# Optimization experiments

Measured on AMD Instinct MI355X. Metric: run time of the kernel, lower is better.

The kernel has to match this reference:

```python
import jax, jax.numpy as jnp
import numpy as np

nA = 4096; nB = 4096; C = 128; H = 4; D = 32; E = 65536
EPS = 1e-5


def _ln(x, g, b):
    m = jnp.mean(x, axis=-1, keepdims=True)
    v = jnp.var(x, axis=-1, keepdims=True)
    return (x - m) / jnp.sqrt(v + EPS) * g + b


def setup_inputs() -> dict:
    key = jax.random.key(0)
    ks = jax.random.split(key, 16)
    w = 0.02
    inp = {}
    inp["x_a"] = jax.random.normal(ks[0], (nA, C), dtype=jnp.float32)
    inp["x_b"] = jax.random.normal(ks[1], (nB, C), dtype=jnp.float32)
    inp["edge_ab"] = jax.random.randint(ks[2], (2, E), 0, nA)  # row0: src in A, row1: dst in B
    inp["edge_ba"] = jax.random.randint(ks[3], (2, E), 0, nB)  # row0: src in B, row1: dst in A
    inp["Wq"] = jax.random.normal(ks[4], (C, C), dtype=jnp.float32) * w
    inp["bq"] = jnp.zeros((C,), jnp.float32)
    inp["Wk"] = jax.random.normal(ks[5], (C, C), dtype=jnp.float32) * w
    inp["bk"] = jnp.zeros((C,), jnp.float32)
    inp["Wv"] = jax.random.normal(ks[6], (C, C), dtype=jnp.float32) * w
    inp["bv"] = jnp.zeros((C,), jnp.float32)
    inp["Wo"] = jax.random.normal(ks[7], (C, C), dtype=jnp.float32) * w
    inp["bo"] = jnp.zeros((C,), jnp.float32)
    inp["g_attn"] = jnp.ones((C,), jnp.float32)   # pre_ln_attn
    inp["b_attn"] = jnp.zeros((C,), jnp.float32)
    inp["g_ffn"] = jnp.ones((C,), jnp.float32)    # pre_ln_ffn
    inp["b_ffn"] = jnp.zeros((C,), jnp.float32)
    inp["g_f"] = jnp.ones((C,), jnp.float32)      # LayerNorm inside ffn Sequential
    inp["b_f"] = jnp.zeros((C,), jnp.float32)
    inp["W1"] = jax.random.normal(ks[8], (C, C), dtype=jnp.float32) * w
    inp["b1"] = jnp.zeros((C,), jnp.float32)
    inp["W2"] = jax.random.normal(ks[9], (C, C), dtype=jnp.float32) * w
    inp["b2"] = jnp.zeros((C,), jnp.float32)
    inp["rel_ab"] = jax.random.normal(ks[10], (1,), dtype=jnp.float32)
    inp["rel_ba"] = jax.random.normal(ks[11], (1,), dtype=jnp.float32)
    return inp


def reference(x_a, x_b, edge_ab, edge_ba, Wq, bq, Wk, bk, Wv, bv, Wo, bo,
              g_attn, b_attn, g_ffn, b_ffn, g_f, b_f, W1, b1, W2, b2,
              rel_ab, rel_ba):
    inv_sqrt_d = 1.0 / jnp.sqrt(jnp.float32(D))

    def all_pairs_attn(xq, xkv, rel):
        nQ, nK = xq.shape[0], xkv.shape[0]
        Q = (xq @ Wq + bq).reshape(nQ, H, D)
        K = (xkv @ Wk + bk).reshape(nK, H, D)
        V = (xkv @ Wv + bv).reshape(nK, H, D)
        # [nQ, nK, H] logits with additive relation bias
        logits = jnp.einsum('ihd,jhd->ijh', Q, K) * inv_sqrt_d + rel
        a = jax.nn.softmax(logits, axis=1)  # softmax over all source nodes per dst
        return jnp.einsum('ijh,jhd->ihd', a, V).reshape(nQ, C)

    xn_a = _ln(x_a, g_attn, b_attn)
    xn_b = _ln(x_b, g_attn, b_attn)
    # edge type B->A contributes to dst type A; A->B to dst type B
    attn_a = all_pairs_attn(xn_a, xn_b, rel_ba[0]) @ Wo + bo
    attn_b = all_pairs_attn(xn_b, xn_a, rel_ab[0]) @ Wo + bo

    # total degree = out-degree + in-degree across edge types (eval: dropout = identity)
    ones = jnp.ones((E,), jnp.float32)
    deg_a = jax.ops.segment_sum(ones, edge_ab[0], num_segments=nA) + \
            jax.ops.segment_sum(ones, edge_ba[1], num_segments=nA)
    deg_b = jax.ops.segment_sum(ones, edge_ba[0], num_segments=nB) + \
            jax.ops.segment_sum(ones, edge_ab[1], num_segments=nB)
    attn_a = attn_a + deg_a[:, None]
    attn_b = attn_b + deg_b[:, None]

    res_a = x_a + attn_a
    res_b = x_b + attn_b

    def ffn(xr):
        h = _ln(xr, g_ffn, b_ffn)        # pre_ln_ffn
        h = _ln(h, g_f, b_f)             # LayerNorm inside ffn Sequential
        h = jax.nn.gelu(h @ W1 + b1, approximate=False)
        return h @ W2 + b2

    out_a = res_a + ffn(res_a)
    out_b = res_b + ffn(res_b)
    return jnp.stack([out_a, out_b])  # [2, n, C]
```

## Files before the change

### kernel.cpp

```cpp
#include <hip/hip_runtime.h>

typedef unsigned short u16;
typedef unsigned int   u32;
typedef __attribute__((ext_vector_type(8))) short bf16x8;
typedef __attribute__((ext_vector_type(4))) float f32x4;

#define NEL (8192*128)

#define ASYNC16(ldsptr, gptr) __builtin_amdgcn_global_load_lds( \
    (const __attribute__((address_space(1))) u32*)(gptr), \
    (__attribute__((address_space(3))) u32*)(ldsptr), 16, 0, 0)

__device__ __forceinline__ u16 f2bf(float f){
  u32 u = __builtin_bit_cast(u32, f);
  u = (u + 0x7FFFu + ((u >> 16) & 1u)) >> 16;
  return (u16)u;
}
__device__ __forceinline__ u32 pk2(float a, float b){
  u32 r;
  asm("v_cvt_pk_bf16_f32 %0, %1, %2" : "=v"(r) : "v"(a), "v"(b));
  return r;
}

__global__ __launch_bounds__(256) void prep_kernel(
    const int* __restrict__ eab, const int* __restrict__ eba, float* __restrict__ deg,
    const float* __restrict__ Wq, const float* __restrict__ Wk, const float* __restrict__ Wv,
    const float* __restrict__ Wo, const float* __restrict__ W1, const float* __restrict__ W2,
    u16* __restrict__ WT)
{
  __shared__ float tile[32][33];
  const int b = blockIdx.x, t = threadIdx.x;
  if (b < 256){
    int e = b*256 + t;
    atomicAdd(&deg[eab[e]],              1.f);
    atomicAdd(&deg[4096 + eab[65536+e]], 1.f);
    atomicAdd(&deg[4096 + eba[e]],       1.f);
    atomicAdd(&deg[eba[65536+e]],        1.f);
  } else {
    int id = b - 256;
    int w = id >> 4, tt = id & 15, tr = tt >> 2, tc = tt & 3;
    const float* W = (w==0)?Wq:(w==1)?Wk:(w==2)?Wv:(w==3)?Wo:(w==4)?W1:W2;
    int r = t >> 3, c4 = (t&7)*4;
    float4 v = *(const float4*)(W + (tr*32 + r)*128 + tc*32 + c4);
    tile[r][c4]=v.x; tile[r][c4+1]=v.y; tile[r][c4+2]=v.z; tile[r][c4+3]=v.w;
    __syncthreads();
    int n = t >> 3, k4 = (t&7)*4;
    u32 lo = pk2(tile[k4+0][n], tile[k4+1][n]);
    u32 hi = pk2(tile[k4+2][n], tile[k4+3][n]);
    *(uint2*)(WT + w*16384 + (tc*32+n)*128 + tr*32 + k4) = make_uint2(lo, hi);
  }
}

__global__ __launch_bounds__(256) void ln_qkv_kernel(
    const float* __restrict__ xa, const float* __restrict__ xb,
    const float* __restrict__ g, const float* __restrict__ bvec,
    const u16* __restrict__ WT,
    const float* __restrict__ bq, const float* __restrict__ bk, const float* __restrict__ bv,
    u16* __restrict__ Qb, u16* __restrict__ Kb, u16* __restrict__ VT)
{
  __shared__ float xs[16][132];
  __shared__ __align__(16) u16 abf[16][128];
  __shared__ __align__(16) u16 vtb[128][24];
  const int t = threadIdx.x, lane = t&63, wave = t>>6;
  const int lq = lane&15, lg = lane>>4;
  const int row0 = blockIdx.x*16;
  const float* x = (row0 < 4096) ? (xa + row0*128) : (xb + (row0-4096)*128);
  #pragma unroll
  for (int i=0;i<2;i++){
    int id = t + i*256; int r = id>>5, c4 = (id&31)*4;
    float4 v = *(const float4*)(x + r*128 + c4);
    xs[r][c4]=v.x; xs[r][c4+1]=v.y; xs[r][c4+2]=v.z; xs[r][c4+3]=v.w;
  }
  __syncthreads();
  {
    int r = t>>4, c0 = t&15;
    float s=0.f, s2=0.f;
    #pragma unroll
    for (int j=0;j<8;j++){ float v = xs[r][c0+j*16]; s+=v; s2+=v*v; }
    #pragma unroll
    for (int m=1;m<16;m<<=1){ s += __shfl_xor(s,m); s2 += __shfl_xor(s2,m); }
    float mean = s*0.0078125f;
    float var  = s2*0.0078125f - mean*mean;
    float rstd = rsqrtf(var + 1e-5f);
    #pragma unroll
    for (int j=0;j<8;j++){
      int c = c0 + j*16;
      float h = (xs[r][c]-mean)*rstd*g[c] + bvec[c];
      int sj = (c>>3) ^ (r&7);
      abf[r][sj*8 + (c&7)] = f2bf(h);
    }
  }
  __syncthreads();
  bf16x8 af[4];
  #pragma unroll
  for (int s=0;s<4;s++){
    int sj = (s*4+lg) ^ (lq&7);
    af[s] = *(const bf16x8*)&abf[lq][sj*8];
  }
  const int cb = wave*32;
  const float QSC = 0.17677669529663687f * 1.4426950408889634f;
  #pragma unroll
  for (int m=0;m<3;m++){
    const u16* Wg = WT + m*16384;
    bf16x8 bf[2][4];
    #pragma unroll
    for (int ct=0;ct<2;ct++)
      #pragma unroll
      for (int s=0;s<4;s++)
        bf[ct][s] = *(const bf16x8*)(Wg + (cb+ct*16+lq)*128 + s*32 + lg*8);
    f32x4 acc[2] = {{0,0,0,0},{0,0,0,0}};
    #pragma unroll
    for (int ct=0;ct<2;ct++)
      #pragma unroll
      for (int s=0;s<4;s++)
        acc[ct] = __builtin_amdgcn_mfma_f32_16x16x32_bf16(af[s], bf[ct][s], acc[ct], 0,0,0);
    #pragma unroll
    for (int ct=0;ct<2;ct++){
      int col = cb + ct*16 + lq;
      if (m==0){
        float bb = bq[col];
        #pragma unroll
        for (int r=0;r<4;r++)
          Qb[(row0+4*lg+r)*128 + col] = f2bf((acc[ct][r]+bb)*QSC);
      } else if (m==1){
        float bb = bk[col];
        #pragma unroll
        for (int r=0;r<4;r++)
          Kb[(row0+4*lg+r)*128 + col] = f2bf(acc[ct][r]+bb);
      } else {
        float bb = bv[col];
        #pragma unroll
        for (int r=0;r<4;r++)
          vtb[col][4*lg+r] = f2bf(acc[ct][r]+bb);
      }
    }
  }
  __syncthreads();
  {
    int c = t>>1, half = t&1;
    bf16x8 v = *(const bf16x8*)&vtb[c][half*8];
    *(bf16x8*)(VT + c*8192 + row0 + half*8) = v;
  }
}

__global__ __launch_bounds__(256) void attn_kernel(
    const u16* __restrict__ Qb, const u16* __restrict__ Kb,
    const u16* __restrict__ VT, float* __restrict__ attnraw)
{
  __shared__ __align__(16) u16 Klds[2][4096];
  __shared__ __align__(16) u16 Vlds[2][4096];
  __shared__ __align__(16) u16 Plds[4][2048];
  const int t = threadIdx.x, wave = t>>6, lane = t&63;
  const int lq = lane&15, lg = lane>>4;
  const int h = blockIdx.y, dir = blockIdx.z;
  const int q = blockIdx.x*64 + wave*16 + lq + (dir ? 4096 : 0);
  const int kvb0 = dir ? 0 : 4096;

  bf16x8 qf = *(const bf16x8*)(Qb + q*128 + h*32 + lg*8);
  f32x4 acc0 = {0,0,0,0}, acc1 = {0,0,0,0}, accL = {0,0,0,0};
  bf16x8 ones;
  #pragma unroll
  for (int i=0;i<8;i++) ones[i] = (short)0x3F80;

  const u16* gk = Kb + (kvb0 + (t>>2))*128 + h*32 + (t&3)*8;
  const u16* gv = VT + (h*32 + (t>>4))*8192 + kvb0 + ((t&15)^(t>>4))*8;

  ASYNC16(&Klds[0][t*8],      gk);
  ASYNC16(&Klds[0][t*8+2048], gk + 8192);
  ASYNC16(&Vlds[0][t*8],      gv);
  ASYNC16(&Vlds[0][t*8+2048], gv + 131072);
  asm volatile("s_waitcnt vmcnt(0)" ::: "memory");
  __builtin_amdgcn_s_barrier();

  int cur = 0;
  for (int kt=0; kt<32; ++kt){
    if (kt < 31){
      gk += 16384; gv += 128;
      int nb = cur^1;
      ASYNC16(&Klds[nb][t*8],      gk);
      ASYNC16(&Klds[nb][t*8+2048], gk + 8192);
      ASYNC16(&Vlds[nb][t*8],      gv);
      ASYNC16(&Vlds[nb][t*8+2048], gv + 131072);
    }
    const u16* KL = Klds[cur];
    const u16* VL = Vlds[cur];
    u16* PL = Plds[wave] + lq*128;
    #pragma unroll
    for (int f=0; f<8; ++f){
      bf16x8 kf = *(const bf16x8*)(KL + (f*16+lq)*32 + lg*8);
      f32x4 st = __builtin_amdgcn_mfma_f32_16x16x32_bf16(kf, qf, (f32x4){0.f,0.f,0.f,0.f}, 0,0,0);
      float p0 = __builtin_amdgcn_exp2f(st[0]);
      float p1 = __builtin_amdgcn_exp2f(st[1]);
      float p2 = __builtin_amdgcn_exp2f(st[2]);
      float p3 = __builtin_amdgcn_exp2f(st[3]);
      int j = f*2 + (lg>>1);
      *(uint2*)(PL + ((j ^ lq)<<3) + (lg&1)*4) = make_uint2(pk2(p0,p1), pk2(p2,p3));
    }
    #pragma unroll
    for (int kc=0; kc<4; ++kc){
      int sj = (kc*4+lg) ^ lq;
      bf16x8 pf  = *(const bf16x8*)(PL + (sj<<3));
      bf16x8 vf0 = *(const bf16x8*)(VL + lq*128      + (sj<<3));
      bf16x8 vf1 = *(const bf16x8*)(VL + (16+lq)*128 + (sj<<3));
      acc0 = __builtin_amdgcn_mfma_f32_16x16x32_bf16(vf0,  pf, acc0, 0,0,0);
      acc1 = __builtin_amdgcn_mfma_f32_16x16x32_bf16(vf1,  pf, acc1, 0,0,0);
      accL = __builtin_amdgcn_mfma_f32_16x16x32_bf16(ones, pf, accL, 0,0,0);
    }
    asm volatile("s_waitcnt vmcnt(0)" ::: "memory");
    __builtin_amdgcn_s_barrier();
    cur ^= 1;
  }
  float inv = __builtin_amdgcn_rcpf(accL[0]);
  float* outp = attnraw + q*128 + h*32 + 4*lg;
  *(float4*)(outp)      = make_float4(acc0[0]*inv, acc0[1]*inv, acc0[2]*inv, acc0[3]*inv);
  *(float4*)(outp + 16) = make_float4(acc1[0]*inv, acc1[1]*inv, acc1[2]*inv, acc1[3]*inv);
}

__global__ __launch_bounds__(256) void tail_kernel(
    const float* __restrict__ attnraw, const u16* __restrict__ WT,
    const float* __restrict__ bo, const float* __restrict__ deg,
    const float* __restrict__ xa, const float* __restrict__ xb,
    const float* __restrict__ gf1, const float* __restrict__ bf1,
    const float* __restrict__ gf2, const float* __restrict__ bf2,
    const float* __restrict__ b1, const float* __restrict__ b2,
    float* __restrict__ out)
{
  __shared__ __align__(16) u16 abf[16][128];
  __shared__ float rs[16][132];
  const int t = threadIdx.x, lane = t&63, wave = t>>6;
  const int lq = lane&15, lg = lane>>4;
  const int row0 = blockIdx.x*16;
  const int cb = wave*32;

  {
    int r = t>>4, j = t&15;
    const float* p = attnraw + (row0+r)*128 + j*8;
    float4 v0 = *(const float4*)(p), v1 = *(const float4*)(p+4);
    bf16x8 bv;
    bv[0]=(short)f2bf(v0.x); bv[1]=(short)f2bf(v0.y); bv[2]=(short)f2bf(v0.z); bv[3]=(short)f2bf(v0.w);
    bv[4]=(short)f2bf(v1.x); bv[5]=(short)f2bf(v1.y); bv[6]=(short)f2bf(v1.z); bv[7]=(short)f2bf(v1.w);
    int sj = j ^ (r&7);
    *(bf16x8*)&abf[r][sj*8] = bv;
  }
  __syncthreads();

  bf16x8 af[4];
  #pragma unroll
  for (int s=0;s<4;s++){ int sj = (s*4+lg) ^ (lq&7); af[s] = *(const bf16x8*)&abf[lq][sj*8]; }

  f32x4 acc[2] = {{0,0,0,0},{0,0,0,0}};
  {
    const u16* Wg = WT + 3*16384;
    bf16x8 bf[2][4];
    #pragma unroll
    for (int ct=0;ct<2;ct++)
      #pragma unroll
      for (int s=0;s<4;s++)
        bf[ct][s] = *(const bf16x8*)(Wg + (cb+ct*16+lq)*128 + s*32 + lg*8);
    #pragma unroll
    for (int ct=0;ct<2;ct++)
      #pragma unroll
      for (int s=0;s<4;s++)
        acc[ct] = __builtin_amdgcn_mfma_f32_16x16x32_bf16(af[s], bf[ct][s], acc[ct], 0,0,0);
  }
  const float* xres = (row0<4096)? (xa + row0*128) : (xb + (row0-4096)*128);
  float rv[2][4];
  #pragma unroll
  for (int ct=0;ct<2;ct++){
    int col = cb + ct*16 + lq;
    float bb = bo[col];
    #pragma unroll
    for (int r=0;r<4;r++){
      int lr = 4*lg + r;
      rv[ct][r] = acc[ct][r] + bb + deg[row0+lr] + xres[lr*128 + col];
      rs[lr][col] = rv[ct][r];
    }
  }
  __syncthreads();
  {
    int r = t>>4, c0 = t&15;
    float s=0.f, s2=0.f;
    #pragma unroll
    for (int j=0;j<8;j++){ float v = rs[r][c0+j*16]; s+=v; s2+=v*v; }
    #pragma unroll
    for (int m=1;m<16;m<<=1){ s += __shfl_xor(s,m); s2 += __shfl_xor(s2,m); }
    float mean = s*0.0078125f;
    float var  = s2*0.0078125f - mean*mean;
    float rstd = rsqrtf(var + 1e-5f);
    float h8[8];
    #pragma unroll
    for (int j=0;j<8;j++){ int c=c0+j*16; h8[j] = (rs[r][c]-mean)*rstd*gf1[c] + bf1[c]; }
    s=0.f; s2=0.f;
    #pragma unroll
    for (int j=0;j<8;j++){ s+=h8[j]; s2+=h8[j]*h8[j]; }
    #pragma unroll
    for (int m=1;m<16;m<<=1){ s += __shfl_xor(s,m); s2 += __shfl_xor(s2,m); }
    float mean2 = s*0.0078125f;
    float var2  = s2*0.0078125f - mean2*mean2;
    float rstd2 = rsqrtf(var2 + 1e-5f);
    #pragma unroll
    for (int j=0;j<8;j++){
      int c = c0 + j*16;
      float h = (h8[j]-mean2)*rstd2*gf2[c] + bf2[c];
      int sj = (c>>3) ^ (r&7);
      abf[r][sj*8 + (c&7)] = f2bf(h);
    }
  }
  __syncthreads();
  #pragma unroll
  for (int s=0;s<4;s++){ int sj = (s*4+lg) ^ (lq&7); af[s] = *(const bf16x8*)&abf[lq][sj*8]; }
  acc[0] = (f32x4){0,0,0,0}; acc[1] = (f32x4){0,0,0,0};
  {
    const u16* Wg = WT + 4*16384;
    bf16x8 bf[2][4];
    #pragma unroll
    for (int ct=0;ct<2;ct++)
      #pragma unroll
      for (int s=0;s<4;s++)
        bf[ct][s] = *(const bf16x8*)(Wg + (cb+ct*16+lq)*128 + s*32 + lg*8);
    #pragma unroll
    for (int ct=0;ct<2;ct++)
      #pragma unroll
      for (int s=0;s<4;s++)
        acc[ct] = __builtin_amdgcn_mfma_f32_16x16x32_bf16(af[s], bf[ct][s], acc[ct], 0,0,0);
  }
  float gvv[2][4];
  #pragma unroll
  for (int ct=0;ct<2;ct++){
    int col = cb + ct*16 + lq;
    float bb = b1[col];
    #pragma unroll
    for (int r=0;r<4;r++){
      float v = acc[ct][r] + bb;
      gvv[ct][r] = 0.5f*v*(1.f + erff(v*0.70710678118654752f));
    }
  }
  __syncthreads();
  #pragma unroll
  for (int ct=0;ct<2;ct++){
    int col = cb + ct*16 + lq;
    #pragma unroll
    for (int r=0;r<4;r++){
      int lr = 4*lg + r;
      int sj = (col>>3) ^ (lr&7);
      abf[lr][sj*8 + (col&7)] = f2bf(gvv[ct][r]);
    }
  }
  __syncthreads();
  #pragma unroll
  for (int s=0;s<4;s++){ int sj = (s*4+lg) ^ (lq&7); af[s] = *(const bf16x8*)&abf[lq][sj*8]; }
  acc[0] = (f32x4){0,0,0,0}; acc[1] = (f32x4){0,0,0,0};
  {
    const u16* Wg = WT + 5*16384;
    bf16x8 bf[2][4];
    #pragma unroll
    for (int ct=0;ct<2;ct++)
      #pragma unroll
      for (int s=0;s<4;s++)
        bf[ct][s] = *(const bf16x8*)(Wg + (cb+ct*16+lq)*128 + s*32 + lg*8);
    #pragma unroll
    for (int ct=0;ct<2;ct++)
      #pragma unroll
      for (int s=0;s<4;s++)
        acc[ct] = __builtin_amdgcn_mfma_f32_16x16x32_bf16(af[s], bf[ct][s], acc[ct], 0,0,0);
  }
  #pragma unroll
  for (int ct=0;ct<2;ct++){
    int col = cb + ct*16 + lq;
    float bb = b2[col];
    #pragma unroll
    for (int r=0;r<4;r++){
      int lr = 4*lg + r;
      out[(row0+lr)*128 + col] = acc[ct][r] + bb + rv[ct][r];
    }
  }
}

extern "C" void kernel_launch(void* const* d_in, const int* in_sizes, int n_in,
                              void* d_out, int out_size, void* d_ws, size_t ws_size,
                              hipStream_t stream) {
  const float* xa  = (const float*)d_in[0];
  const float* xb  = (const float*)d_in[1];
  const int*   eab = (const int*)d_in[2];
  const int*   eba = (const int*)d_in[3];
  const float* Wq  = (const float*)d_in[4];   const float* bq = (const float*)d_in[5];
  const float* Wk  = (const float*)d_in[6];   const float* bk = (const float*)d_in[7];
  const float* Wv  = (const float*)d_in[8];   const float* bv = (const float*)d_in[9];
  const float* Wo  = (const float*)d_in[10];  const float* bo = (const float*)d_in[11];
  const float* ga  = (const float*)d_in[12];  const float* ba = (const float*)d_in[13];
  const float* gfn = (const float*)d_in[14];  const float* bfn= (const float*)d_in[15];
  const float* gf  = (const float*)d_in[16];  const float* bf = (const float*)d_in[17];
  const float* W1  = (const float*)d_in[18];  const float* b1 = (const float*)d_in[19];
  const float* W2  = (const float*)d_in[20];  const float* b2 = (const float*)d_in[21];
  float* out = (float*)d_out;

  char* w = (char*)d_ws;
  float* deg     = (float*)w;
  u16*   WT      = (u16*)(w + 32768);
  u16*   Qb      = (u16*)(w + 32768 + 196608);
  u16*   Kb      = Qb + NEL;
  u16*   VT      = Kb + NEL;
  float* attnraw = (float*)(VT + NEL);

  hipMemsetAsync(deg, 0, 8192*sizeof(float), stream);
  prep_kernel<<<352, 256, 0, stream>>>(eab, eba, deg, Wq, Wk, Wv, Wo, W1, W2, WT);
  ln_qkv_kernel<<<512, 256, 0, stream>>>(xa, xb, ga, ba, WT, bq, bk, bv, Qb, Kb, VT);
  attn_kernel<<<dim3(64,4,2), 256, 0, stream>>>(Qb, Kb, VT, attnraw);
  tail_kernel<<<512, 256, 0, stream>>>(attnraw, WT, bo, deg, xa, xb,
                                       gfn, bfn, gf, bf, b1, b2, out);
}
```

Before: 195.3 us.

## Split attention over key chunks and widen LN/QKV and tail blocks to 512 threads

The attention kernel now splits the 4096 keys into four chunks of 1024 across extra grid blocks. It writes unnormalized partial numerators and denominators, which the tail kernel sums and normalizes. The grid grows from 512 to 2048 blocks to fill more CUs, and K/V LDS tiles are halved with a new XOR swizzle. ln_qkv and tail now use 512 threads, each wave computing 16 output columns instead of 32. This costs extra global traffic for the four partial buffers and an extra reduction in the tail.

New measurement: 184.3 us. 1.06x faster.

```diff
diff --git a/kernel.cpp b/kernel.cpp
--- a/kernel.cpp
+++ b/kernel.cpp
@@ -51,7 +51,7 @@
   }
 }
 
-__global__ __launch_bounds__(256) void ln_qkv_kernel(
+__global__ __launch_bounds__(512) void ln_qkv_kernel(
     const float* __restrict__ xa, const float* __restrict__ xb,
     const float* __restrict__ g, const float* __restrict__ bvec,
     const u16* __restrict__ WT,
@@ -65,14 +65,13 @@
   const int lq = lane&15, lg = lane>>4;
   const int row0 = blockIdx.x*16;
   const float* x = (row0 < 4096) ? (xa + row0*128) : (xb + (row0-4096)*128);
-  #pragma unroll
-  for (int i=0;i<2;i++){
-    int id = t + i*256; int r = id>>5, c4 = (id&31)*4;
+  {
+    int r = t>>5, c4 = (t&31)*4;
     float4 v = *(const float4*)(x + r*128 + c4);
     xs[r][c4]=v.x; xs[r][c4+1]=v.y; xs[r][c4+2]=v.z; xs[r][c4+3]=v.w;
   }
   __syncthreads();
-  {
+  if (t < 256){
     int r = t>>4, c0 = t&15;
     float s=0.f, s2=0.f;
     #pragma unroll
@@ -97,46 +96,39 @@
     int sj = (s*4+lg) ^ (lq&7);
     af[s] = *(const bf16x8*)&abf[lq][sj*8];
   }
-  const int cb = wave*32;
+  const int cb = wave*16;
   const float QSC = 0.17677669529663687f * 1.4426950408889634f;
   #pragma unroll
   for (int m=0;m<3;m++){
     const u16* Wg = WT + m*16384;
-    bf16x8 bf[2][4];
-    #pragma unroll
-    for (int ct=0;ct<2;ct++)
+    bf16x8 bfr[4];
+    #pragma unroll
+    for (int s=0;s<4;s++)
+      bfr[s] = *(const bf16x8*)(Wg + (cb+lq)*128 + s*32 + lg*8);
+    f32x4 acc = {0,0,0,0};
+    #pragma unroll
+    for (int s=0;s<4;s++)
+      acc = __builtin_amdgcn_mfma_f32_16x16x32_bf16(af[s], bfr[s], acc, 0,0,0);
+    int col = cb + lq;
+    if (m==0){
+      float bb = bq[col];
       #pragma unroll
-      for (int s=0;s<4;s++)
-        bf[ct][s] = *(const bf16x8*)(Wg + (cb+ct*16+lq)*128 + s*32 + lg*8);
-    f32x4 acc[2] = {{0,0,0,0},{0,0,0,0}};
-    #pragma unroll
-    for (int ct=0;ct<2;ct++)
+      for (int r=0;r<4;r++)
+        Qb[(row0+4*lg+r)*128 + col] = f2bf((acc[r]+bb)*QSC);
+    } else if (m==1){
+      float bb = bk[col];
       #pragma unroll
-      for (int s=0;s<4;s++)
-        acc[ct] = __builtin_amdgcn_mfma_f32_16x16x32_bf16(af[s], bf[ct][s], acc[ct], 0,0,0);
-    #pragma unroll
-    for (int ct=0;ct<2;ct++){
-      int col = cb + ct*16 + lq;
-      if (m==0){
-        float bb = bq[col];
-        #pragma unroll
-        for (int r=0;r<4;r++)
-          Qb[(row0+4*lg+r)*128 + col] = f2bf((acc[ct][r]+bb)*QSC);
-      } else if (m==1){
-        float bb = bk[col];
-        #pragma unroll
-        for (int r=0;r<4;r++)
-          Kb[(row0+4*lg+r)*128 + col] = f2bf(acc[ct][r]+bb);
-      } else {
-        float bb = bv[col];
-        #pragma unroll
-        for (int r=0;r<4;r++)
-          vtb[col][4*lg+r] = f2bf(acc[ct][r]+bb);
-      }
-    }
-  }
-  __syncthreads();
-  {
+      for (int r=0;r<4;r++)
+        Kb[(row0+4*lg+r)*128 + col] = f2bf(acc[r]+bb);
+    } else {
+      float bb = bv[col];
+      #pragma unroll
+      for (int r=0;r<4;r++)
+        vtb[col][4*lg+r] = f2bf(acc[r]+bb);
+    }
+  }
+  __syncthreads();
+  if (t < 256){
     int c = t>>1, half = t&1;
     bf16x8 v = *(const bf16x8*)&vtb[c][half*8];
     *(bf16x8*)(VT + c*8192 + row0 + half*8) = v;
@@ -145,16 +137,17 @@
 
 __global__ __launch_bounds__(256) void attn_kernel(
     const u16* __restrict__ Qb, const u16* __restrict__ Kb,
-    const u16* __restrict__ VT, float* __restrict__ attnraw)
+    const u16* __restrict__ VT, float* __restrict__ numb, float* __restrict__ denb)
 {
-  __shared__ __align__(16) u16 Klds[2][4096];
-  __shared__ __align__(16) u16 Vlds[2][4096];
-  __shared__ __align__(16) u16 Plds[4][2048];
+  __shared__ __align__(16) u16 Klds[2][2048];
+  __shared__ __align__(16) u16 Vlds[2][2048];
+  __shared__ __align__(16) u16 Plds[4][1024];
   const int t = threadIdx.x, wave = t>>6, lane = t&63;
   const int lq = lane&15, lg = lane>>4;
-  const int h = blockIdx.y, dir = blockIdx.z;
+  const int h = blockIdx.y;
+  const int dir = blockIdx.z >> 2, sp = blockIdx.z & 3;
   const int q = blockIdx.x*64 + wave*16 + lq + (dir ? 4096 : 0);
-  const int kvb0 = dir ? 0 : 4096;
+  const int kvb = (dir ? 0 : 4096) + sp*1024;
 
   bf16x8 qf = *(const bf16x8*)(Qb + q*128 + h*32 + lg*8);
   f32x4 acc0 = {0,0,0,0}, acc1 = {0,0,0,0}, accL = {0,0,0,0};
@@ -162,46 +155,42 @@
   #pragma unroll
   for (int i=0;i<8;i++) ones[i] = (short)0x3F80;
 
-  const u16* gk = Kb + (kvb0 + (t>>2))*128 + h*32 + (t&3)*8;
-  const u16* gv = VT + (h*32 + (t>>4))*8192 + kvb0 + ((t&15)^(t>>4))*8;
-
-  ASYNC16(&Klds[0][t*8],      gk);
-  ASYNC16(&Klds[0][t*8+2048], gk + 8192);
-  ASYNC16(&Vlds[0][t*8],      gv);
-  ASYNC16(&Vlds[0][t*8+2048], gv + 131072);
+  const u16* gk = Kb + (kvb + (t>>2))*128 + h*32 + ((t&3) ^ ((t>>3)&3))*8;
+  const u16* gv = VT + (h*32 + (t>>3))*8192 + kvb + ((t&7) ^ ((t>>3)&7))*8;
+
+  ASYNC16(&Klds[0][t*8], gk);
+  ASYNC16(&Vlds[0][t*8], gv);
   asm volatile("s_waitcnt vmcnt(0)" ::: "memory");
   __builtin_amdgcn_s_barrier();
 
   int cur = 0;
-  for (int kt=0; kt<32; ++kt){
-    if (kt < 31){
-      gk += 16384; gv += 128;
-      int nb = cur^1;
-      ASYNC16(&Klds[nb][t*8],      gk);
-      ASYNC16(&Klds[nb][t*8+2048], gk + 8192);
-      ASYNC16(&Vlds[nb][t*8],      gv);
-      ASYNC16(&Vlds[nb][t*8+2048], gv + 131072);
+  for (int kt=0; kt<16; ++kt){
+    if (kt < 15){
+      gk += 8192; gv += 64;
+      ASYNC16(&Klds[cur^1][t*8], gk);
+      ASYNC16(&Vlds[cur^1][t*8], gv);
     }
     const u16* KL = Klds[cur];
     const u16* VL = Vlds[cur];
-    u16* PL = Plds[wave] + lq*128;
-    #pragma unroll
-    for (int f=0; f<8; ++f){
-      bf16x8 kf = *(const bf16x8*)(KL + (f*16+lq)*32 + lg*8);
+    u16* PL = Plds[wave] + lq*64;
+    const int ksj = lg ^ ((lq>>1)&3);
+    #pragma unroll
+    for (int f=0; f<4; ++f){
+      bf16x8 kf = *(const bf16x8*)(KL + (f*16+lq)*32 + ksj*8);
       f32x4 st = __builtin_amdgcn_mfma_f32_16x16x32_bf16(kf, qf, (f32x4){0.f,0.f,0.f,0.f}, 0,0,0);
       float p0 = __builtin_amdgcn_exp2f(st[0]);
       float p1 = __builtin_amdgcn_exp2f(st[1]);
       float p2 = __builtin_amdgcn_exp2f(st[2]);
       float p3 = __builtin_amdgcn_exp2f(st[3]);
       int j = f*2 + (lg>>1);
-      *(uint2*)(PL + ((j ^ lq)<<3) + (lg&1)*4) = make_uint2(pk2(p0,p1), pk2(p2,p3));
-    }
-    #pragma unroll
-    for (int kc=0; kc<4; ++kc){
-      int sj = (kc*4+lg) ^ lq;
+      *(uint2*)(PL + ((j ^ (lq&7))<<3) + (lg&1)*4) = make_uint2(pk2(p0,p1), pk2(p2,p3));
+    }
+    #pragma unroll
+    for (int kc=0; kc<2; ++kc){
+      int sj = (kc*4+lg) ^ (lq&7);
       bf16x8 pf  = *(const bf16x8*)(PL + (sj<<3));
-      bf16x8 vf0 = *(const bf16x8*)(VL + lq*128      + (sj<<3));
-      bf16x8 vf1 = *(const bf16x8*)(VL + (16+lq)*128 + (sj<<3));
+      bf16x8 vf0 = *(const bf16x8*)(VL + lq*64      + (sj<<3));
+      bf16x8 vf1 = *(const bf16x8*)(VL + (16+lq)*64 + (sj<<3));
       acc0 = __builtin_amdgcn_mfma_f32_16x16x32_bf16(vf0,  pf, acc0, 0,0,0);
       acc1 = __builtin_amdgcn_mfma_f32_16x16x32_bf16(vf1,  pf, acc1, 0,0,0);
       accL = __builtin_amdgcn_mfma_f32_16x16x32_bf16(ones, pf, accL, 0,0,0);
@@ -210,14 +199,15 @@
     __builtin_amdgcn_s_barrier();
     cur ^= 1;
   }
-  float inv = __builtin_amdgcn_rcpf(accL[0]);
-  float* outp = attnraw + q*128 + h*32 + 4*lg;
-  *(float4*)(outp)      = make_float4(acc0[0]*inv, acc0[1]*inv, acc0[2]*inv, acc0[3]*inv);
-  *(float4*)(outp + 16) = make_float4(acc1[0]*inv, acc1[1]*inv, acc1[2]*inv, acc1[3]*inv);
-}
-
-__global__ __launch_bounds__(256) void tail_kernel(
-    const float* __restrict__ attnraw, const u16* __restrict__ WT,
+  float* outp = numb + sp*NEL + q*128 + h*32 + 4*lg;
+  *(float4*)(outp)      = make_float4(acc0[0], acc0[1], acc0[2], acc0[3]);
+  *(float4*)(outp + 16) = make_float4(acc1[0], acc1[1], acc1[2], acc1[3]);
+  if (lg == 0) denb[sp*32768 + q*4 + h] = accL[0];
+}
+
+__global__ __launch_bounds__(512) void tail_kernel(
+    const float* __restrict__ numb, const float* __restrict__ denb,
+    const u16* __restrict__ WT,
     const float* __restrict__ bo, const float* __restrict__ deg,
     const float* __restrict__ xa, const float* __restrict__ xb,
     const float* __restrict__ gf1, const float* __restrict__ bf1,
@@ -230,17 +220,24 @@
   const int t = threadIdx.x, lane = t&63, wave = t>>6;
   const int lq = lane&15, lg = lane>>4;
   const int row0 = blockIdx.x*16;
-  const int cb = wave*32;
-
-  {
-    int r = t>>4, j = t&15;
-    const float* p = attnraw + (row0+r)*128 + j*8;
-    float4 v0 = *(const float4*)(p), v1 = *(const float4*)(p+4);
-    bf16x8 bv;
-    bv[0]=(short)f2bf(v0.x); bv[1]=(short)f2bf(v0.y); bv[2]=(short)f2bf(v0.z); bv[3]=(short)f2bf(v0.w);
-    bv[4]=(short)f2bf(v1.x); bv[5]=(short)f2bf(v1.y); bv[6]=(short)f2bf(v1.z); bv[7]=(short)f2bf(v1.w);
-    int sj = j ^ (r&7);
-    *(bf16x8*)&abf[r][sj*8] = bv;
+  const int cb = wave*16;
+
+  {
+    int r = t>>5, c0 = (t&31)*4, hh = c0>>5;
+    const float* np = numb + (row0+r)*128 + c0;
+    float4 s0 = *(const float4*)(np);
+    float4 s1 = *(const float4*)(np + NEL);
+    float4 s2 = *(const float4*)(np + 2*NEL);
+    float4 s3 = *(const float4*)(np + 3*NEL);
+    int di = (row0+r)*4 + hh;
+    float den = denb[di] + denb[32768+di] + denb[65536+di] + denb[98304+di];
+    float inv = 1.0f/den;
+    float a0 = (s0.x+s1.x+s2.x+s3.x)*inv;
+    float a1 = (s0.y+s1.y+s2.y+s3.y)*inv;
+    float a2 = (s0.z+s1.z+s2.z+s3.z)*inv;
+    float a3 = (s0.w+s1.w+s2.w+s3.w)*inv;
+    int sj = (c0>>3) ^ (r&7);
+    *(uint2*)&abf[r][sj*8 + (c0&7)] = make_uint2(pk2(a0,a1), pk2(a2,a3));
   }
   __syncthreads();
 
@@ -248,36 +245,29 @@
   #pragma unroll
   for (int s=0;s<4;s++){ int sj = (s*4+lg) ^ (lq&7); af[s] = *(const bf16x8*)&abf[lq][sj*8]; }
 
-  f32x4 acc[2] = {{0,0,0,0},{0,0,0,0}};
+  f32x4 acc = {0,0,0,0};
   {
     const u16* Wg = WT + 3*16384;
-    bf16x8 bf[2][4];
-    #pragma unroll
-    for (int ct=0;ct<2;ct++)
-      #pragma unroll
-      for (int s=0;s<4;s++)
-        bf[ct][s] = *(const bf16x8*)(Wg + (cb+ct*16+lq)*128 + s*32 + lg*8);
-    #pragma unroll
-    for (int ct=0;ct<2;ct++)
-      #pragma unroll
-      for (int s=0;s<4;s++)
-        acc[ct] = __builtin_amdgcn_mfma_f32_16x16x32_bf16(af[s], bf[ct][s], acc[ct], 0,0,0);
+    bf16x8 bfr[4];
+    #pragma unroll
+    for (int s=0;s<4;s++) bfr[s] = *(const bf16x8*)(Wg + (cb+lq)*128 + s*32 + lg*8);
+    #pragma unroll
+    for (int s=0;s<4;s++) acc = __builtin_amdgcn_mfma_f32_16x16x32_bf16(af[s], bfr[s], acc, 0,0,0);
   }
   const float* xres = (row0<4096)? (xa + row0*128) : (xb + (row0-4096)*128);
-  float rv[2][4];
-  #pragma unroll
-  for (int ct=0;ct<2;ct++){
-    int col = cb + ct*16 + lq;
+  const int col = cb + lq;
+  float rv[4];
+  {
     float bb = bo[col];
     #pragma unroll
     for (int r=0;r<4;r++){
       int lr = 4*lg + r;
-      rv[ct][r] = acc[ct][r] + bb + deg[row0+lr] + xres[lr*128 + col];
-      rs[lr][col] = rv[ct][r];
-    }
-  }
-  __syncthreads();
-  {
+      rv[r] = acc[r] + bb + deg[row0+lr] + xres[lr*128 + col];
+      rs[lr][col] = rv[r];
+    }
+  }
+  __syncthreads();
+  if (t < 256){
     int r = t>>4, c0 = t&15;
     float s=0.f, s2=0.f;
     #pragma unroll
@@ -309,69 +299,49 @@
   __syncthreads();
   #pragma unroll
   for (int s=0;s<4;s++){ int sj = (s*4+lg) ^ (lq&7); af[s] = *(const bf16x8*)&abf[lq][sj*8]; }
-  acc[0] = (f32x4){0,0,0,0}; acc[1] = (f32x4){0,0,0,0};
+  acc = (f32x4){0,0,0,0};
   {
     const u16* Wg = WT + 4*16384;
-    bf16x8 bf[2][4];
-    #pragma unroll
-    for (int ct=0;ct<2;ct++)
-      #pragma unroll
-      for (int s=0;s<4;s++)
-        bf[ct][s] = *(const bf16x8*)(Wg + (cb+ct*16+lq)*128 + s*32 + lg*8);
-    #pragma unroll
-    for (int ct=0;ct<2;ct++)
-      #pragma unroll
-      for (int s=0;s<4;s++)
-        acc[ct] = __builtin_amdgcn_mfma_f32_16x16x32_bf16(af[s], bf[ct][s], acc[ct], 0,0,0);
-  }
-  float gvv[2][4];
-  #pragma unroll
-  for (int ct=0;ct<2;ct++){
-    int col = cb + ct*16 + lq;
+    bf16x8 bfr[4];
+    #pragma unroll
+    for (int s=0;s<4;s++) bfr[s] = *(const bf16x8*)(Wg + (cb+lq)*128 + s*32 + lg*8);
+    #pragma unroll
+    for (int s=0;s<4;s++) acc = __builtin_amdgcn_mfma_f32_16x16x32_bf16(af[s], bfr[s], acc, 0,0,0);
+  }
+  float gvv[4];
+  {
     float bb = b1[col];
     #pragma unroll
     for (int r=0;r<4;r++){
-      float v = acc[ct][r] + bb;
-      gvv[ct][r] = 0.5f*v*(1.f + erff(v*0.70710678118654752f));
-    }
-  }
-  __syncthreads();
-  #pragma unroll
-  for (int ct=0;ct<2;ct++){
-    int col = cb + ct*16 + lq;
+      float v = acc[r] + bb;
+      gvv[r] = 0.5f*v*(1.f + erff(v*0.70710678118654752f));
+    }
+  }
+  __syncthreads();
+  #pragma unroll
+  for (int r=0;r<4;r++){
+    int lr = 4*lg + r;
+    int sj = (col>>3) ^ (lr&7);
+    abf[lr][sj*8 + (col&7)] = f2bf(gvv[r]);
+  }
+  __syncthreads();
+  #pragma unroll
+  for (int s=0;s<4;s++){ int sj = (s*4+lg) ^ (lq&7); af[s] = *(const bf16x8*)&abf[lq][sj*8]; }
+  acc = (f32x4){0,0,0,0};
+  {
+    const u16* Wg = WT + 5*16384;
+    bf16x8 bfr[4];
+    #pragma unroll
+    for (int s=0;s<4;s++) bfr[s] = *(const bf16x8*)(Wg + (cb+lq)*128 + s*32 + lg*8);
+    #pragma unroll
+    for (int s=0;s<4;s++) acc = __builtin_amdgcn_mfma_f32_16x16x32_bf16(af[s], bfr[s], acc, 0,0,0);
+  }
+  {
+    float bb = b2[col];
     #pragma unroll
     for (int r=0;r<4;r++){
       int lr = 4*lg + r;
-      int sj = (col>>3) ^ (lr&7);
-      abf[lr][sj*8 + (col&7)] = f2bf(gvv[ct][r]);
-    }
-  }
-  __syncthreads();
-  #pragma unroll
-  for (int s=0;s<4;s++){ int sj = (s*4+lg) ^ (lq&7); af[s] = *(const bf16x8*)&abf[lq][sj*8]; }
-  acc[0] = (f32x4){0,0,0,0}; acc[1] = (f32x4){0,0,0,0};
-  {
-    const u16* Wg = WT + 5*16384;
-    bf16x8 bf[2][4];
-    #pragma unroll
-    for (int ct=0;ct<2;ct++)
-      #pragma unroll
-      for (int s=0;s<4;s++)
-        bf[ct][s] = *(const bf16x8*)(Wg + (cb+ct*16+lq)*128 + s*32 + lg*8);
-    #pragma unroll
-    for (int ct=0;ct<2;ct++)
-      #pragma unroll
-      for (int s=0;s<4;s++)
-        acc[ct] = __builtin_amdgcn_mfma_f32_16x16x32_bf16(af[s], bf[ct][s], acc[ct], 0,0,0);
-  }
-  #pragma unroll
-  for (int ct=0;ct<2;ct++){
-    int col = cb + ct*16 + lq;
-    float bb = b2[col];
-    #pragma unroll
-    for (int r=0;r<4;r++){
-      int lr = 4*lg + r;
-      out[(row0+lr)*128 + col] = acc[ct][r] + bb + rv[ct][r];
+      out[(row0+lr)*128 + col] = acc[r] + bb + rv[r];
     }
   }
 }
@@ -395,17 +365,18 @@
   float* out = (float*)d_out;
 
   char* w = (char*)d_ws;
-  float* deg     = (float*)w;
-  u16*   WT      = (u16*)(w + 32768);
-  u16*   Qb      = (u16*)(w + 32768 + 196608);
-  u16*   Kb      = Qb + NEL;
-  u16*   VT      = Kb + NEL;
-  float* attnraw = (float*)(VT + NEL);
+  float* deg  = (float*)w;
+  u16*   WT   = (u16*)(w + 32768);
+  u16*   Qb   = (u16*)(w + 32768 + 196608);
+  u16*   Kb   = Qb + NEL;
+  u16*   VT   = Kb + NEL;
+  float* numb = (float*)(VT + NEL);
+  float* denb = numb + 4*NEL;
 
   hipMemsetAsync(deg, 0, 8192*sizeof(float), stream);
   prep_kernel<<<352, 256, 0, stream>>>(eab, eba, deg, Wq, Wk, Wv, Wo, W1, W2, WT);
-  ln_qkv_kernel<<<512, 256, 0, stream>>>(xa, xb, ga, ba, WT, bq, bk, bv, Qb, Kb, VT);
-  attn_kernel<<<dim3(64,4,2), 256, 0, stream>>>(Qb, Kb, VT, attnraw);
-  tail_kernel<<<512, 256, 0, stream>>>(attnraw, WT, bo, deg, xa, xb,
+  ln_qkv_kernel<<<512, 512, 0, stream>>>(xa, xb, ga, ba, WT, bq, bk, bv, Qb, Kb, VT);
+  attn_kernel<<<dim3(64,4,8), 256, 0, stream>>>(Qb, Kb, VT, numb, denb);
+  tail_kernel<<<512, 512, 0, stream>>>(numb, denb, WT, bo, deg, xa, xb,
                                        gfn, bfn, gf, bf, b1, b2, out);
 }
```
